# Kernel tuning notes

Hardware: AMD Instinct MI355X
Metric: run time of the kernel (lower is better)

The kernel has to match this reference:

```python
import jax, jax.numpy as jnp
import numpy as np
from jax import lax

DIM = 384
HEADS = 8
PROMPTDIM = 192
EPS = 1e-12  # torch F.normalize eps


def conv1x1(x, w):
    # x: [b,c,h,w], w: [out,c]
    return jnp.einsum('bchw,oc->bohw', x, w)


def dwconv3x3(x, w):
    # depthwise 3x3, SAME padding; w: [C,1,3,3]
    return lax.conv_general_dilated(
        x, w, window_strides=(1, 1), padding='SAME',
        feature_group_count=x.shape[1],
        dimension_numbers=('NCHW', 'OIHW', 'NCHW'))


def setup_inputs() -> dict:
    key = jax.random.key(0)
    ks = jax.random.split(key, 8)
    b, h, w = 8, 128, 128
    s = 0.05
    return {
        'x': jax.random.normal(ks[0], (b, DIM, h, w), jnp.float32),
        'de': jax.random.normal(ks[1], (b, PROMPTDIM, h, w), jnp.float32),
        'w_qv': jax.random.normal(ks[2], (2 * DIM, DIM), jnp.float32) * s,
        'w_qv_dw': jax.random.normal(ks[3], (2 * DIM, 1, 3, 3), jnp.float32) * s,
        'w_k': jax.random.normal(ks[4], (DIM, PROMPTDIM), jnp.float32) * s,
        'w_k_dw': jax.random.normal(ks[5], (DIM, 1, 3, 3), jnp.float32) * s,
        'w_proj': jax.random.normal(ks[6], (DIM, DIM), jnp.float32) * s,
        'temperature': jnp.ones((HEADS, 1, 1), jnp.float32),
    }


def reference(x, de, w_qv, w_qv_dw, w_k, w_k_dw, w_proj, temperature):
    b, c, h, w = x.shape
    head_c = c // HEADS
    qv = dwconv3x3(conv1x1(x, w_qv), w_qv_dw)          # [b,2c,h,w]
    q, v = qv[:, :c], qv[:, c:]
    k = dwconv3x3(conv1x1(de, w_k), w_k_dw)            # [b,c,h,w]

    def to_heads(t):
        return t.reshape(b, HEADS, head_c, h * w)       # [b,head,c,hw]

    q, k, v = to_heads(q), to_heads(k), to_heads(v)
    # L2-normalize over hw (torch F.normalize: x / max(||x||, eps))
    q = q / jnp.maximum(jnp.linalg.norm(q, axis=-1, keepdims=True), EPS)
    k = k / jnp.maximum(jnp.linalg.norm(k, axis=-1, keepdims=True), EPS)
    attn = jnp.einsum('bhcs,bhds->bhcd', q, k) * temperature  # [b,head,c,c]
    attn = jax.nn.softmax(attn, axis=-1)
    out = jnp.einsum('bhcd,bhds->bhcs', attn, v)        # [b,head,c,hw]
    out = out.reshape(b, c, h, w)
    return conv1x1(out, w_proj)
```

## Files before the change

kernel.cpp:

```cpp
#include <hip/hip_runtime.h>

#define SPATIAL 16384
#define BATCH 8
#define CDIM 384
#define QVDIM 768
#define PDIM 192
#define NHEADS 8
#define HC 48

typedef __attribute__((ext_vector_type(8))) short short8;
typedef __attribute__((ext_vector_type(4))) float f32x4;
typedef __attribute__((ext_vector_type(4))) int i32x4;

__device__ __forceinline__ unsigned short f2bf(float f) {
  union { float f; unsigned u; } v; v.f = f;
  unsigned r = v.u + 0x7fffu + ((v.u >> 16) & 1u);
  return (unsigned short)(r >> 16);
}
__device__ __forceinline__ float bf2f(unsigned short h) {
  union { unsigned u; float f; } v; v.u = ((unsigned)h) << 16;
  return v.f;
}

__device__ __forceinline__ void gload16(const unsigned short* g, unsigned short* lds) {
  __builtin_amdgcn_global_load_lds(
      (const __attribute__((address_space(1))) void*)g,
      (__attribute__((address_space(3))) void*)lds,
      16, 0, 0);
}

__global__ void k_w2bf(const float* __restrict__ in, unsigned short* __restrict__ out, int n) {
  int i = blockIdx.x * 256 + threadIdx.x;
  if (i < n) out[i] = f2bf(in[i]);
}

__global__ __launch_bounds__(256)
void k_transpose(const float* __restrict__ in, unsigned short* __restrict__ out, int C) {
  __shared__ float tile[64][65];
  int bid = blockIdx.x;
  int st = bid % (SPATIAL / 64); bid /= (SPATIAL / 64);
  int ct = bid % (C / 64); int b = bid / (C / 64);
  int t = threadIdx.x;
  const float* ip = in + ((size_t)b * C + (size_t)ct * 64) * SPATIAL + (size_t)st * 64;
  int fx = t & 15, fy = t >> 4;
#pragma unroll
  for (int i = 0; i < 4; i++) {
    int r = fy + i * 16;
    f32x4 v = *(const f32x4*)(ip + (size_t)r * SPATIAL + fx * 4);
    tile[r][fx * 4 + 0] = v[0];
    tile[r][fx * 4 + 1] = v[1];
    tile[r][fx * 4 + 2] = v[2];
    tile[r][fx * 4 + 3] = v[3];
  }
  __syncthreads();
  unsigned short* op = out + ((size_t)b * SPATIAL + (size_t)st * 64) * C + (size_t)ct * 64;
  int cg = t & 7, sr = t >> 3;
#pragma unroll
  for (int i = 0; i < 2; i++) {
    int s = sr + i * 32;
    short8 o;
#pragma unroll
    for (int j = 0; j < 8; j++) o[j] = (short)f2bf(tile[cg * 8 + j][s]);
    *(short8*)(op + (size_t)s * C + cg * 8) = o;
  }
}

template<int BM, bool OUT_BF16>
__global__ __launch_bounds__(512, 2)
void k_gemm(const unsigned short* __restrict__ A, const unsigned short* __restrict__ B,
            void* __restrict__ Cv, int M, int K, long strideA)
{
  constexpr int MFR = BM / 32;
  constexpr int AR  = BM / 128;
  constexpr int SL  = AR + 2;
  constexpr int ASZ = BM * 32;
  constexpr int BUF = ASZ + 256 * 32;

  int nwg = gridDim.x;
  int bid = (blockIdx.x & 7) * (nwg >> 3) + (blockIdx.x >> 3);
  int mt = M / BM;
  int mb = bid % mt; bid /= mt;
  int nb = bid & 63; int b = bid >> 6;

  const unsigned short* Ab = A + (size_t)b * strideA + (size_t)mb * BM * K;
  const unsigned short* Bb = B + ((size_t)b * SPATIAL + (size_t)nb * 256) * K;

  __shared__ unsigned short lds[2 * BUF];

  int t = threadIdx.x;
  int lane = t & 63;
  int w = t >> 6;
  int wm = (w >> 2) * (BM / 2), wn = (w & 3) * 64;
  int lr = lane & 15, lg = lane >> 4;
  int colr = (lg ^ ((lr >> 1) & 3)) * 8;

  f32x4 acc[MFR][4];
#pragma unroll
  for (int i = 0; i < MFR; i++)
#pragma unroll
    for (int j = 0; j < 4; j++)
      acc[i][j] = (f32x4){0.f, 0.f, 0.f, 0.f};

  int arow0 = t >> 2;
  int aslot = (t & 3) ^ ((arow0 >> 1) & 3);
  const unsigned short* gA0 = Ab + (size_t)arow0 * K + aslot * 8;
  const unsigned short* gB0 = Bb + (size_t)arow0 * K + aslot * 8;

  auto STAGE = [&](int kt, int q) {
    int k0 = kt * 32;
    unsigned short* base = &lds[q * BUF];
#pragma unroll
    for (int r2 = 0; r2 < AR; ++r2)
      gload16(gA0 + (size_t)r2 * 128 * K + k0, base + r2 * 4096 + w * 512);
#pragma unroll
    for (int r2 = 0; r2 < 2; ++r2)
      gload16(gB0 + (size_t)r2 * 128 * K + k0, base + ASZ + r2 * 4096 + w * 512);
  };

  int nt = K >> 5;
  STAGE(0, 0);
  STAGE(1, 1);
  asm volatile("s_waitcnt vmcnt(%0)" :: "n"(SL) : "memory");
  __builtin_amdgcn_sched_barrier(0);

  for (int j = 0; j < nt; ++j) {
    unsigned short* cb = &lds[(j & 1) * BUF];
    __builtin_amdgcn_s_barrier();
    __builtin_amdgcn_sched_barrier(0);

    short8 af[MFR], bfv[4];
#pragma unroll
    for (int mi = 0; mi < MFR; ++mi)
      af[mi] = *(const short8*)(&cb[(wm + mi * 16 + lr) * 32 + colr]);
#pragma unroll
    for (int ni = 0; ni < 4; ++ni)
      bfv[ni] = *(const short8*)(&cb[ASZ + (wn + ni * 16 + lr) * 32 + colr]);

    asm volatile("s_waitcnt lgkmcnt(0)" ::: "memory");
    __builtin_amdgcn_sched_barrier(0);
    __builtin_amdgcn_s_barrier();
    if (j + 2 < nt) STAGE(j + 2, j & 1);

    __builtin_amdgcn_s_setprio(1);
#pragma unroll
    for (int mi = 0; mi < MFR; ++mi)
#pragma unroll
      for (int ni = 0; ni < 4; ++ni)
        acc[mi][ni] = __builtin_amdgcn_mfma_f32_16x16x32_bf16(af[mi], bfv[ni], acc[mi][ni], 0, 0, 0);
    __builtin_amdgcn_s_setprio(0);
    __builtin_amdgcn_sched_barrier(0);

    if (j + 2 < nt) {
      asm volatile("s_waitcnt vmcnt(%0)" :: "n"(SL) : "memory");
    } else if (j + 1 < nt) {
      asm volatile("s_waitcnt vmcnt(0)" ::: "memory");
    }
    __builtin_amdgcn_sched_barrier(0);
  }

  size_t rbase = (size_t)mb * BM + wm + lg * 4;
  size_t cbase = (size_t)nb * 256 + wn + lr;
  if (OUT_BF16) {
    unsigned short* C = (unsigned short*)Cv + (size_t)b * M * SPATIAL;
#pragma unroll
    for (int mi = 0; mi < MFR; ++mi)
#pragma unroll
      for (int ni = 0; ni < 4; ++ni) {
        size_t r = rbase + mi * 16;
        size_t c = cbase + ni * 16;
#pragma unroll
        for (int jj = 0; jj < 4; ++jj)
          C[(r + jj) * SPATIAL + c] = f2bf(acc[mi][ni][jj]);
      }
  } else {
    float* C = (float*)Cv + (size_t)b * M * SPATIAL;
#pragma unroll
    for (int mi = 0; mi < MFR; ++mi)
#pragma unroll
      for (int ni = 0; ni < 4; ++ni) {
        size_t r = rbase + mi * 16;
        size_t c = cbase + ni * 16;
#pragma unroll
        for (int jj = 0; jj < 4; ++jj)
          C[(r + jj) * SPATIAL + c] = acc[mi][ni][jj];
      }
  }
}

template<bool NORM>
__global__ __launch_bounds__(256)
void k_dwconv(const unsigned short* __restrict__ in, const float* __restrict__ wdw,
              unsigned short* __restrict__ out, float* __restrict__ norm2,
              int C, int in_cstride, int chan_off)
{
  int bid = blockIdx.x;
  int yt = bid & 7; bid >>= 3;
  int c = bid % C; int b = bid / C;
  const unsigned short* ip = in + ((size_t)b * in_cstride + chan_off + c) * SPATIAL;
  const float* wp = wdw + (size_t)(chan_off + c) * 9;
  float wr[9];
#pragma unroll
  for (int i = 0; i < 9; i++) wr[i] = wp[i];

  int t = threadIdx.x;
  int ty = t >> 4, xs = (t & 15) * 8;
  int y = yt * 16 + ty;

  float acc[8];
#pragma unroll
  for (int j = 0; j < 8; j++) acc[j] = 0.f;

  auto row = [&](int yy, float wa, float wb, float wc) {
    if ((unsigned)yy >= 128u) return;
    const unsigned short* rp = ip + yy * 128 + xs;
    short8 cv = *(const short8*)rp;
    float cf[8];
#pragma unroll
    for (int j = 0; j < 8; j++) cf[j] = bf2f((unsigned short)cv[j]);
    float lf = (xs > 0) ? bf2f(rp[-1]) : 0.f;
    float rt = (xs < 120) ? bf2f(rp[8]) : 0.f;
    acc[0] += wa * lf + wb * cf[0] + wc * cf[1];
#pragma unroll
    for (int j = 1; j < 7; j++) acc[j] += wa * cf[j - 1] + wb * cf[j] + wc * cf[j + 1];
    acc[7] += wa * cf[6] + wb * cf[7] + wc * rt;
  };
  row(y - 1, wr[0], wr[1], wr[2]);
  row(y,     wr[3], wr[4], wr[5]);
  row(y + 1, wr[6], wr[7], wr[8]);

  short8 o;
  float sq = 0.f;
#pragma unroll
  for (int j = 0; j < 8; j++) {
    o[j] = (short)f2bf(acc[j]);
    if (NORM) { float v = bf2f((unsigned short)o[j]); sq += v * v; }
  }
  *(short8*)(out + ((size_t)b * C + c) * SPATIAL + y * 128 + xs) = o;

  if (NORM) {
#pragma unroll
    for (int off = 32; off > 0; off >>= 1) sq += __shfl_down(sq, off, 64);
    __shared__ float red[4];
    if ((t & 63) == 0) red[t >> 6] = sq;
    __syncthreads();
    if (t == 0)
      atomicAdd(&norm2[(size_t)b * C + c], red[0] + red[1] + red[2] + red[3]);
  }
}

__global__ __launch_bounds__(256)
void k_dwconv_t(const unsigned short* __restrict__ qv, const float* __restrict__ wdw,
                unsigned short* __restrict__ vT)
{
  __shared__ float tile[128][17];
  int bid = blockIdx.x;
  int y = bid & 127; bid >>= 7;
  int ct = bid % 24; int b = bid / 24;
  int t = threadIdx.x;
  int ci = t >> 4, xs = (t & 15) * 8;
  int c = CDIM + ct * 16 + ci;
  const unsigned short* ip = qv + ((size_t)b * QVDIM + c) * SPATIAL;
  const float* wp = wdw + (size_t)c * 9;
  float wr[9];
#pragma unroll
  for (int i = 0; i < 9; i++) wr[i] = wp[i];

  float acc[8];
#pragma unroll
  for (int j = 0; j < 8; j++) acc[j] = 0.f;

  auto row = [&](int yy, float wa, float wb, float wc) {
    if ((unsigned)yy >= 128u) return;
    const unsigned short* rp = ip + yy * 128 + xs;
    short8 cv = *(const short8*)rp;
    float cf[8];
#pragma unroll
    for (int j = 0; j < 8; j++) cf[j] = bf2f((unsigned short)cv[j]);
    float lf = (xs > 0) ? bf2f(rp[-1]) : 0.f;
    float rt = (xs < 120) ? bf2f(rp[8]) : 0.f;
    acc[0] += wa * lf + wb * cf[0] + wc * cf[1];
#pragma unroll
    for (int j = 1; j < 7; j++) acc[j] += wa * cf[j - 1] + wb * cf[j] + wc * cf[j + 1];
    acc[7] += wa * cf[6] + wb * cf[7] + wc * rt;
  };
  row(y - 1, wr[0], wr[1], wr[2]);
  row(y,     wr[3], wr[4], wr[5]);
  row(y + 1, wr[6], wr[7], wr[8]);

#pragma unroll
  for (int j = 0; j < 8; j++) tile[xs + j][ci] = acc[j];
  __syncthreads();

  int xw = t >> 1, cg = t & 1;
  short8 o;
#pragma unroll
  for (int j = 0; j < 8; j++) o[j] = (short)f2bf(tile[xw][cg * 8 + j]);
  *(short8*)(vT + ((size_t)b * SPATIAL + (size_t)y * 128 + xw) * CDIM + ct * 16 + cg * 8) = o;
}

__global__ __launch_bounds__(256)
void k_logits(const unsigned short* __restrict__ qd, const unsigned short* __restrict__ kd,
              float* __restrict__ raw)
{
  int bid = blockIdx.x;
  int sp = bid & 15; bid >>= 4;
  int h = bid & 7; int b = bid >> 3;
  int lane = threadIdx.x & 63, wv = threadIdx.x >> 6;
  int lr = lane & 15, lg = lane >> 4;
  const unsigned short* qp = qd + ((size_t)b * CDIM + h * HC) * SPATIAL;
  const unsigned short* kp = kd + ((size_t)b * CDIM + h * HC) * SPATIAL;
  int s0 = sp * 1024 + wv * 256;
  f32x4 acc[3][3];
#pragma unroll
  for (int i = 0; i < 3; i++)
#pragma unroll
    for (int j = 0; j < 3; j++)
      acc[i][j] = (f32x4){0.f, 0.f, 0.f, 0.f};
  for (int ks = 0; ks < 256; ks += 32) {
    int off = s0 + ks + lg * 8;
    short8 qf[3], kf[3];
#pragma unroll
    for (int i = 0; i < 3; i++) {
      qf[i] = *(const short8*)(qp + (size_t)(i * 16 + lr) * SPATIAL + off);
      kf[i] = *(const short8*)(kp + (size_t)(i * 16 + lr) * SPATIAL + off);
    }
#pragma unroll
    for (int ci = 0; ci < 3; ci++)
#pragma unroll
      for (int di = 0; di < 3; di++)
        acc[ci][di] = __builtin_amdgcn_mfma_f32_16x16x32_bf16(qf[ci], kf[di], acc[ci][di], 0, 0, 0);
  }
  float* rp = raw + ((size_t)(b * NHEADS + h)) * HC * HC;
#pragma unroll
  for (int ci = 0; ci < 3; ci++)
#pragma unroll
    for (int di = 0; di < 3; di++)
#pragma unroll
      for (int j = 0; j < 4; j++)
        atomicAdd(&rp[(ci * 16 + lg * 4 + j) * HC + di * 16 + lr], acc[ci][di][j]);
}

__global__ void k_softmax(const float* __restrict__ raw, const float* __restrict__ n2q,
                          const float* __restrict__ n2k, const float* __restrict__ temp,
                          float* __restrict__ attn)
{
  int h = blockIdx.x & 7, b = blockIdx.x >> 3;
  int c = threadIdx.x;
  if (c >= HC) return;
  float tp = temp[h];
  float qn = fmaxf(sqrtf(n2q[b * CDIM + h * HC + c]), 1e-12f);
  const float* rp = raw + ((size_t)(b * NHEADS + h) * HC + c) * HC;
  float vals[HC];
  float mx = -1e30f;
#pragma unroll
  for (int d = 0; d < HC; d++) {
    float kn = fmaxf(sqrtf(n2k[b * CDIM + h * HC + d]), 1e-12f);
    float v = rp[d] * tp / (qn * kn);
    vals[d] = v;
    mx = fmaxf(mx, v);
  }
  float sum = 0.f;
#pragma unroll
  for (int d = 0; d < HC; d++) { vals[d] = expf(vals[d] - mx); sum += vals[d]; }
  float inv = 1.f / sum;
  float* ap = attn + ((size_t)(b * NHEADS + h) * HC + c) * HC;
#pragma unroll
  for (int d = 0; d < HC; d++) ap[d] = vals[d] * inv;
}

__global__ void k_mbuild(const float* __restrict__ attn, const float* __restrict__ wproj,
                         unsigned short* __restrict__ Mb)
{
  int o = blockIdx.x % CDIM, b = blockIdx.x / CDIM;
  int j = threadIdx.x;
  int h = j / HC, d = j % HC;
  const float* wp = wproj + (size_t)o * CDIM + h * HC;
  const float* ap = attn + (size_t)(b * NHEADS + h) * HC * HC + d;
  float s = 0.f;
#pragma unroll
  for (int cp = 0; cp < HC; cp++) s += wp[cp] * ap[cp * HC];
  Mb[((size_t)b * CDIM + o) * CDIM + j] = f2bf(s);
}

static const size_t OFF_QV   = 0;
static const size_t OFF_KDW  = 0;
static const size_t OFF_XT   = 201326592;
static const size_t OFF_QDW  = 201326592;
static const size_t OFF_DET  = 301989888;
static const size_t OFF_VT   = 301989888;
static const size_t OFF_KPRE = 402653184;
static const size_t OFF_WQVB = 503316480;
static const size_t OFF_WKB  = 503906304;
static const size_t OFF_N2Q  = 504053760;
static const size_t OFF_N2K  = 504066048;
static const size_t OFF_RAW  = 504078336;
static const size_t OFF_ATTN = 504668160;
static const size_t OFF_MB   = 505257984;

extern "C" void kernel_launch(void* const* d_in, const int* in_sizes, int n_in,
                              void* d_out, int out_size, void* d_ws, size_t ws_size,
                              hipStream_t stream) {
  const float* x      = (const float*)d_in[0];
  const float* de     = (const float*)d_in[1];
  const float* w_qv   = (const float*)d_in[2];
  const float* w_qvdw = (const float*)d_in[3];
  const float* w_k    = (const float*)d_in[4];
  const float* w_kdw  = (const float*)d_in[5];
  const float* w_proj = (const float*)d_in[6];
  const float* temp   = (const float*)d_in[7];

  char* ws = (char*)d_ws;
  unsigned short* qv    = (unsigned short*)(ws + OFF_QV);
  unsigned short* kdw   = (unsigned short*)(ws + OFF_KDW);
  unsigned short* xT    = (unsigned short*)(ws + OFF_XT);
  unsigned short* qdw   = (unsigned short*)(ws + OFF_QDW);
  unsigned short* deT   = (unsigned short*)(ws + OFF_DET);
  unsigned short* vT    = (unsigned short*)(ws + OFF_VT);
  unsigned short* kpre  = (unsigned short*)(ws + OFF_KPRE);
  unsigned short* wqvb  = (unsigned short*)(ws + OFF_WQVB);
  unsigned short* wkb   = (unsigned short*)(ws + OFF_WKB);
  float* n2q  = (float*)(ws + OFF_N2Q);
  float* n2k  = (float*)(ws + OFF_N2K);
  float* raw  = (float*)(ws + OFF_RAW);
  float* attn = (float*)(ws + OFF_ATTN);
  unsigned short* Mb = (unsigned short*)(ws + OFF_MB);

  hipMemsetAsync(ws + OFF_N2Q, 0, 12288 + 12288 + 589824, stream);

  k_w2bf<<<dim3((QVDIM * CDIM + 255) / 256), dim3(256), 0, stream>>>(w_qv, wqvb, QVDIM * CDIM);
  k_w2bf<<<dim3((CDIM * PDIM + 255) / 256), dim3(256), 0, stream>>>(w_k, wkb, CDIM * PDIM);

  k_transpose<<<dim3(BATCH * (CDIM / 64) * (SPATIAL / 64)), dim3(256), 0, stream>>>(x, xT, CDIM);
  k_transpose<<<dim3(BATCH * (PDIM / 64) * (SPATIAL / 64)), dim3(256), 0, stream>>>(de, deT, PDIM);

  k_gemm<256, true><<<dim3(BATCH * (QVDIM / 256) * (SPATIAL / 256)), dim3(512), 0, stream>>>(
      wqvb, xT, (void*)qv, QVDIM, CDIM, 0L);
  k_gemm<128, true><<<dim3(BATCH * (CDIM / 128) * (SPATIAL / 256)), dim3(512), 0, stream>>>(
      wkb, deT, (void*)kpre, CDIM, PDIM, 0L);

  k_dwconv<true><<<dim3(BATCH * CDIM * 8), dim3(256), 0, stream>>>(
      qv, w_qvdw, qdw, n2q, CDIM, QVDIM, 0);
  k_dwconv_t<<<dim3(BATCH * 24 * 128), dim3(256), 0, stream>>>(qv, w_qvdw, vT);
  k_dwconv<true><<<dim3(BATCH * CDIM * 8), dim3(256), 0, stream>>>(
      kpre, w_kdw, kdw, n2k, CDIM, CDIM, 0);

  k_logits<<<dim3(BATCH * NHEADS * 16), dim3(256), 0, stream>>>(qdw, kdw, raw);
  k_softmax<<<dim3(BATCH * NHEADS), dim3(64), 0, stream>>>(raw, n2q, n2k, temp, attn);
  k_mbuild<<<dim3(BATCH * CDIM), dim3(CDIM), 0, stream>>>(attn, w_proj, Mb);

  k_gemm<128, false><<<dim3(BATCH * (CDIM / 128) * (SPATIAL / 256)), dim3(512), 0, stream>>>(
      Mb, vT, d_out, CDIM, CDIM, (long)(CDIM * CDIM));
}
```

Baseline: 661.9 us.

## Triple-buffer LDS and prefetch next fragments into registers during MFMA

Moves the GEMM main loop from double to triple LDS buffering, keeping three K-tiles of global loads in flight. It also ping-pongs register fragments, so the LDS reads for tile j+1 are issued before the MFMAs for tile j run, hiding LDS latency behind matrix work. In exchange, LDS use per block grows by half and more registers are live, which may lower occupancy. The loop steps by two tiles, so it assumes nt is even.

```diff
diff --git a/kernel.cpp b/kernel.cpp
--- a/kernel.cpp
+++ b/kernel.cpp
@@ -85,7 +85,7 @@
   const unsigned short* Ab = A + (size_t)b * strideA + (size_t)mb * BM * K;
   const unsigned short* Bb = B + ((size_t)b * SPATIAL + (size_t)nb * 256) * K;
 
-  __shared__ unsigned short lds[2 * BUF];
+  __shared__ unsigned short lds[3 * BUF];
 
   int t = threadIdx.x;
   int lane = t & 63;
@@ -118,45 +118,56 @@
   };
 
   int nt = K >> 5;
-  STAGE(0, 0);
-  STAGE(1, 1);
-  asm volatile("s_waitcnt vmcnt(%0)" :: "n"(SL) : "memory");
+  STAGE(0, 0); STAGE(1, 1); STAGE(2, 2);
+  asm volatile("s_waitcnt vmcnt(%0)" :: "n"(2 * SL) : "memory");
+  __builtin_amdgcn_s_barrier();
   __builtin_amdgcn_sched_barrier(0);
 
-  for (int j = 0; j < nt; ++j) {
-    unsigned short* cb = &lds[(j & 1) * BUF];
-    __builtin_amdgcn_s_barrier();
-    __builtin_amdgcn_sched_barrier(0);
-
-    short8 af[MFR], bfv[4];
+  short8 afA[MFR], bfA[4], afB[MFR], bfB[4];
+  {
+    unsigned short* cb = &lds[0];
 #pragma unroll
     for (int mi = 0; mi < MFR; ++mi)
-      af[mi] = *(const short8*)(&cb[(wm + mi * 16 + lr) * 32 + colr]);
+      afA[mi] = *(const short8*)(&cb[(wm + mi * 16 + lr) * 32 + colr]);
 #pragma unroll
     for (int ni = 0; ni < 4; ++ni)
-      bfv[ni] = *(const short8*)(&cb[ASZ + (wn + ni * 16 + lr) * 32 + colr]);
-
-    asm volatile("s_waitcnt lgkmcnt(0)" ::: "memory");
-    __builtin_amdgcn_sched_barrier(0);
-    __builtin_amdgcn_s_barrier();
-    if (j + 2 < nt) STAGE(j + 2, j & 1);
-
-    __builtin_amdgcn_s_setprio(1);
-#pragma unroll
-    for (int mi = 0; mi < MFR; ++mi)
-#pragma unroll
-      for (int ni = 0; ni < 4; ++ni)
-        acc[mi][ni] = __builtin_amdgcn_mfma_f32_16x16x32_bf16(af[mi], bfv[ni], acc[mi][ni], 0, 0, 0);
-    __builtin_amdgcn_s_setprio(0);
-    __builtin_amdgcn_sched_barrier(0);
-
-    if (j + 2 < nt) {
-      asm volatile("s_waitcnt vmcnt(%0)" :: "n"(SL) : "memory");
-    } else if (j + 1 < nt) {
-      asm volatile("s_waitcnt vmcnt(0)" ::: "memory");
-    }
-    __builtin_amdgcn_sched_barrier(0);
-  }
+      bfA[ni] = *(const short8*)(&cb[ASZ + (wn + ni * 16 + lr) * 32 + colr]);
+  }
+
+#define GBODY(AFM, BFM, AFR, BFR)                                             \
+  {                                                                           \
+    asm volatile("s_waitcnt lgkmcnt(0)" ::: "memory");                        \
+    __builtin_amdgcn_sched_barrier(0);                                        \
+    if (j + 2 < nt) { asm volatile("s_waitcnt vmcnt(%0)" :: "n"(SL) : "memory"); } \
+    else            { asm volatile("s_waitcnt vmcnt(0)" ::: "memory"); }      \
+    __builtin_amdgcn_s_barrier();                                             \
+    __builtin_amdgcn_sched_barrier(0);                                        \
+    if (j + 3 < nt) STAGE(j + 3, j % 3);                                      \
+    if (j + 1 < nt) {                                                         \
+      unsigned short* cb = &lds[((j + 1) % 3) * BUF];                         \
+      _Pragma("unroll")                                                       \
+      for (int mi = 0; mi < MFR; ++mi)                                        \
+        AFR[mi] = *(const short8*)(&cb[(wm + mi * 16 + lr) * 32 + colr]);     \
+      _Pragma("unroll")                                                       \
+      for (int ni = 0; ni < 4; ++ni)                                          \
+        BFR[ni] = *(const short8*)(&cb[ASZ + (wn + ni * 16 + lr) * 32 + colr]); \
+    }                                                                         \
+    __builtin_amdgcn_sched_barrier(0);                                        \
+    __builtin_amdgcn_s_setprio(1);                                            \
+    _Pragma("unroll")                                                         \
+    for (int mi = 0; mi < MFR; ++mi)                                          \
+      _Pragma("unroll")                                                       \
+      for (int ni = 0; ni < 4; ++ni)                                          \
+        acc[mi][ni] = __builtin_amdgcn_mfma_f32_16x16x32_bf16(AFM[mi], BFM[ni], acc[mi][ni], 0, 0, 0); \
+    __builtin_amdgcn_s_setprio(0);                                            \
+    __builtin_amdgcn_sched_barrier(0);                                        \
+  }
+
+  for (int jj = 0; jj < nt; jj += 2) {
+    { int j = jj;     GBODY(afA, bfA, afB, bfB) }
+    { int j = jj + 1; GBODY(afB, bfB, afA, bfA) }
+  }
+#undef GBODY
 
   size_t rbase = (size_t)mb * BM + wm + lg * 4;
   size_t cbase = (size_t)nb * 256 + wn + lr;
```

After: 695.3 us. +5.1%, slower.

## Double GEMM K-tile to 64 with 8-slot XOR swizzle and two MFMA sub-steps

Applied to the files above, without the earlier changes.

The bf16 MFMA GEMM now stages 64-wide K tiles instead of 32, halving the number of main-loop iterations and their barriers. The LDS layout moves to an 8-slot XOR swizzle, and each iteration runs two MFMA sub-steps, each on its own 32-wide half. The vmcnt wait is now issued at the top of the loop. LDS use per block doubles, which may reduce occupancy under launch_bounds(512,2), and with less prefetch slack in-flight loads could be exposed.

```diff
diff --git a/kernel.cpp b/kernel.cpp
--- a/kernel.cpp
+++ b/kernel.cpp
@@ -71,10 +71,10 @@
             void* __restrict__ Cv, int M, int K, long strideA)
 {
   constexpr int MFR = BM / 32;
-  constexpr int AR  = BM / 128;
-  constexpr int SL  = AR + 2;
-  constexpr int ASZ = BM * 32;
-  constexpr int BUF = ASZ + 256 * 32;
+  constexpr int ARD = BM / 64;
+  constexpr int SL  = ARD + 4;
+  constexpr int ASZ = BM * 64;
+  constexpr int BUF = ASZ + 256 * 64;
 
   int nwg = gridDim.x;
   int bid = (blockIdx.x & 7) * (nwg >> 3) + (blockIdx.x >> 3);
@@ -92,7 +92,6 @@
   int w = t >> 6;
   int wm = (w >> 2) * (BM / 2), wn = (w & 3) * 64;
   int lr = lane & 15, lg = lane >> 4;
-  int colr = (lg ^ ((lr >> 1) & 3)) * 8;
 
   f32x4 acc[MFR][4];
 #pragma unroll
@@ -101,61 +100,73 @@
     for (int j = 0; j < 4; j++)
       acc[i][j] = (f32x4){0.f, 0.f, 0.f, 0.f};
 
-  int arow0 = t >> 2;
-  int aslot = (t & 3) ^ ((arow0 >> 1) & 3);
-  const unsigned short* gA0 = Ab + (size_t)arow0 * K + aslot * 8;
-  const unsigned short* gB0 = Bb + (size_t)arow0 * K + aslot * 8;
+  int arow = t >> 3;
+  int aslot = (t & 7) ^ (arow & 7);
+  const unsigned short* gA0 = Ab + (size_t)arow * K + aslot * 8;
+  const unsigned short* gB0 = Bb + (size_t)arow * K + aslot * 8;
 
   auto STAGE = [&](int kt, int q) {
-    int k0 = kt * 32;
+    int k0 = kt * 64;
     unsigned short* base = &lds[q * BUF];
 #pragma unroll
-    for (int r2 = 0; r2 < AR; ++r2)
-      gload16(gA0 + (size_t)r2 * 128 * K + k0, base + r2 * 4096 + w * 512);
-#pragma unroll
-    for (int r2 = 0; r2 < 2; ++r2)
-      gload16(gB0 + (size_t)r2 * 128 * K + k0, base + ASZ + r2 * 4096 + w * 512);
+    for (int r = 0; r < ARD; ++r)
+      gload16(gA0 + (size_t)r * 64 * K + k0, base + r * 4096 + w * 512);
+#pragma unroll
+    for (int r = 0; r < 4; ++r)
+      gload16(gB0 + (size_t)r * 64 * K + k0, base + ASZ + r * 4096 + w * 512);
   };
 
-  int nt = K >> 5;
+  int nt = K >> 6;
   STAGE(0, 0);
   STAGE(1, 1);
-  asm volatile("s_waitcnt vmcnt(%0)" :: "n"(SL) : "memory");
-  __builtin_amdgcn_sched_barrier(0);
+
+  int colr0 = ((0 * 4 + lg) ^ (lr & 7)) * 8;
+  int colr1 = ((1 * 4 + lg) ^ (lr & 7)) * 8;
 
   for (int j = 0; j < nt; ++j) {
-    unsigned short* cb = &lds[(j & 1) * BUF];
+    if (j + 1 < nt) { asm volatile("s_waitcnt vmcnt(%0)" :: "n"(SL) : "memory"); }
+    else            { asm volatile("s_waitcnt vmcnt(0)" ::: "memory"); }
     __builtin_amdgcn_s_barrier();
     __builtin_amdgcn_sched_barrier(0);
 
-    short8 af[MFR], bfv[4];
-#pragma unroll
-    for (int mi = 0; mi < MFR; ++mi)
-      af[mi] = *(const short8*)(&cb[(wm + mi * 16 + lr) * 32 + colr]);
-#pragma unroll
-    for (int ni = 0; ni < 4; ++ni)
-      bfv[ni] = *(const short8*)(&cb[ASZ + (wn + ni * 16 + lr) * 32 + colr]);
-
-    asm volatile("s_waitcnt lgkmcnt(0)" ::: "memory");
+    unsigned short* cb = &lds[(j & 1) * BUF];
+
+    {
+      short8 af[MFR], bfv[4];
+#pragma unroll
+      for (int mi = 0; mi < MFR; ++mi)
+        af[mi] = *(const short8*)(&cb[(wm + mi * 16 + lr) * 64 + colr0]);
+#pragma unroll
+      for (int ni = 0; ni < 4; ++ni)
+        bfv[ni] = *(const short8*)(&cb[ASZ + (wn + ni * 16 + lr) * 64 + colr0]);
+      __builtin_amdgcn_s_setprio(1);
+#pragma unroll
+      for (int mi = 0; mi < MFR; ++mi)
+#pragma unroll
+        for (int ni = 0; ni < 4; ++ni)
+          acc[mi][ni] = __builtin_amdgcn_mfma_f32_16x16x32_bf16(af[mi], bfv[ni], acc[mi][ni], 0, 0, 0);
+      __builtin_amdgcn_s_setprio(0);
+    }
+    __builtin_amdgcn_sched_barrier(0);
+    {
+      short8 af[MFR], bfv[4];
+#pragma unroll
+      for (int mi = 0; mi < MFR; ++mi)
+        af[mi] = *(const short8*)(&cb[(wm + mi * 16 + lr) * 64 + colr1]);
+#pragma unroll
+      for (int ni = 0; ni < 4; ++ni)
+        bfv[ni] = *(const short8*)(&cb[ASZ + (wn + ni * 16 + lr) * 64 + colr1]);
+      __builtin_amdgcn_s_setprio(1);
+#pragma unroll
+      for (int mi = 0; mi < MFR; ++mi)
+#pragma unroll
+        for (int ni = 0; ni < 4; ++ni)
+          acc[mi][ni] = __builtin_amdgcn_mfma_f32_16x16x32_bf16(af[mi], bfv[ni], acc[mi][ni], 0, 0, 0);
+      __builtin_amdgcn_s_setprio(0);
+    }
     __builtin_amdgcn_sched_barrier(0);
     __builtin_amdgcn_s_barrier();
     if (j + 2 < nt) STAGE(j + 2, j & 1);
-
-    __builtin_amdgcn_s_setprio(1);
-#pragma unroll
-    for (int mi = 0; mi < MFR; ++mi)
-#pragma unroll
-      for (int ni = 0; ni < 4; ++ni)
-        acc[mi][ni] = __builtin_amdgcn_mfma_f32_16x16x32_bf16(af[mi], bfv[ni], acc[mi][ni], 0, 0, 0);
-    __builtin_amdgcn_s_setprio(0);
-    __builtin_amdgcn_sched_barrier(0);
-
-    if (j + 2 < nt) {
-      asm volatile("s_waitcnt vmcnt(%0)" :: "n"(SL) : "memory");
-    } else if (j + 1 < nt) {
-      asm volatile("s_waitcnt vmcnt(0)" ::: "memory");
-    }
-    __builtin_amdgcn_sched_barrier(0);
   }
 
   size_t rbase = (size_t)mb * BM + wm + lg * 4;
```

Result: no change. 660.2 us (-0.3%).
